# Optimization experiments

Measured on AMD Instinct MI355X. Metric: run time of the kernel, lower is better.

Reference implementation:

```python
import jax, jax.numpy as jnp
import numpy as np
from jax import lax

TAU = 1.0
LAMBDA_CONTRAST = 1.0
GAMMA_ALIGN = 1.0
EPSILON = 0.1
SINKHORN_ITERS = 50
B, V_EN, V_CN, K, H, D = 512, 30000, 20000, 100, 512, 300


def setup_inputs() -> dict:
    key = jax.random.key(0)
    ks = jax.random.split(key, 24)
    s = lambda fan_in: 1.0 / np.sqrt(fan_in)
    inp = {
        'x_bow_en': jax.random.uniform(ks[0], (B, V_EN), jnp.float32),
        'x_bow_cn': jax.random.uniform(ks[1], (B, V_CN), jnp.float32),
        'cluster_ids': jax.random.randint(ks[2], (B,), 0, 9, jnp.int32),
        'eps_en': jax.random.normal(ks[3], (B, K), jnp.float32),
        'eps_cn': jax.random.normal(ks[4], (B, K), jnp.float32),
        # English encoder params
        'W1_en': jax.random.normal(ks[5], (V_EN, H), jnp.float32) * s(V_EN),
        'b1_en': jnp.zeros((H,), jnp.float32),
        'W2_en': jax.random.normal(ks[6], (H, H), jnp.float32) * s(H),
        'b2_en': jnp.zeros((H,), jnp.float32),
        'Wmu_en': jax.random.normal(ks[7], (H, K), jnp.float32) * s(H),
        'bmu_en': jnp.zeros((K,), jnp.float32),
        'Wlv_en': jax.random.normal(ks[8], (H, K), jnp.float32) * s(H),
        'blv_en': jnp.zeros((K,), jnp.float32),
        # Chinese encoder params
        'W1_cn': jax.random.normal(ks[9], (V_CN, H), jnp.float32) * s(V_CN),
        'b1_cn': jnp.zeros((H,), jnp.float32),
        'W2_cn': jax.random.normal(ks[10], (H, H), jnp.float32) * s(H),
        'b2_cn': jnp.zeros((H,), jnp.float32),
        'Wmu_cn': jax.random.normal(ks[11], (H, K), jnp.float32) * s(H),
        'bmu_cn': jnp.zeros((K,), jnp.float32),
        'Wlv_cn': jax.random.normal(ks[12], (H, K), jnp.float32) * s(H),
        'blv_cn': jnp.zeros((K,), jnp.float32),
        # frozen word embeddings + topic embeddings
        'word_emb_en': jax.random.normal(ks[13], (V_EN, D), jnp.float32),
        'word_emb_cn': jax.random.normal(ks[14], (V_CN, D), jnp.float32),
        'topic_emb': jax.random.normal(ks[15], (K, D), jnp.float32),
    }
    return inp


def _encoder(x, eps, W1, b1, W2, b2, Wmu, bmu, Wlv, blv):
    h = jax.nn.softplus(x @ W1 + b1)
    h = jax.nn.softplus(h @ W2 + b2)
    mu = h @ Wmu + bmu
    logvar = h @ Wlv + blv
    z = mu + eps * jnp.exp(0.5 * logvar)  # reparameterization
    theta = jax.nn.softmax(z, axis=-1)
    return theta, mu, logvar


def _compute_beta(word_emb, topic_emb, tau):
    # torch.cdist p=2 -> euclidean distance [V, K]
    sq = (jnp.sum(word_emb ** 2, -1)[:, None] + jnp.sum(topic_emb ** 2, -1)[None, :]
          - 2.0 * word_emb @ topic_emb.T)
    dist = jnp.sqrt(jnp.maximum(sq, 0.0))
    beta = jnp.exp(-dist / tau)
    beta = beta / jnp.sum(beta, axis=0, keepdims=True)  # normalize over vocab
    return beta.T  # [K, V]


def _tm_loss(x_bow, theta, beta, mu, logvar):
    recon = theta @ beta  # [B, V]
    recon_loss = jnp.mean(-jnp.sum(x_bow * jax.nn.log_softmax(recon, axis=-1), axis=-1))
    kl = jnp.mean(0.5 * jnp.sum(jnp.exp(logvar) + mu ** 2 - 1.0 - logvar, axis=-1))
    return recon_loss + kl


def _contrastive_loss(theta_en, theta_cn, cluster_ids, tau):
    b = theta_en.shape[0]
    parity = (jnp.arange(b) % 2 == 0)[:, None]
    thetas = jnp.where(parity, theta_en, theta_cn)  # anchor/other selection
    tn = thetas / jnp.maximum(jnp.linalg.norm(thetas, axis=-1, keepdims=True), 1e-8)
    E = jnp.exp((tn @ tn.T) / tau)  # exp(cos_sim / tau), [B, B]
    offdiag = ~jnp.eye(b, dtype=bool)
    valid = cluster_ids > 0  # falsy cluster -> skipped, matching torch truthiness
    same = cluster_ids[:, None] == cluster_ids[None, :]
    pos_mask = offdiag & same & valid[:, None] & valid[None, :]
    pos_sim = jnp.sum(jnp.where(pos_mask, E, 0.0), axis=1)
    neg_sum = jnp.sum(jnp.where(offdiag, E, 0.0), axis=1)  # all j != i
    has_pos = valid & (jnp.sum(pos_mask, axis=1) > 0)
    per = -jnp.log(pos_sim / (pos_sim + neg_sum + 1e-8))
    loss = jnp.sum(jnp.where(has_pos, per, 0.0))
    count = jnp.sum(has_pos).astype(jnp.float32)
    return loss / (count + 1e-8)


def _sinkhorn(a, b, C, eps):
    Kmat = jnp.exp(-C / eps)
    def step(uv, _):
        u, v = uv
        u = a / (Kmat @ v + 1e-8)
        v = b / (Kmat.T @ u + 1e-8)
        return (u, v), None
    (u, v), _ = lax.scan(step, (jnp.ones_like(a), jnp.ones_like(b)), None, length=SINKHORN_ITERS)
    return u[:, None] * Kmat * v[None, :]


def _alignment_loss(topic_emb, eps):
    tn = topic_emb / jnp.maximum(jnp.linalg.norm(topic_emb, axis=-1, keepdims=True), 1e-8)
    C = 1.0 - tn @ tn.T
    k = topic_emb.shape[0]
    a = jnp.full((k,), 1.0 / k, jnp.float32)
    Q = _sinkhorn(a, a, C, eps)
    return jnp.sum(Q * C)


def reference(x_bow_en, x_bow_cn, cluster_ids, eps_en, eps_cn,
              W1_en, b1_en, W2_en, b2_en, Wmu_en, bmu_en, Wlv_en, blv_en,
              W1_cn, b1_cn, W2_cn, b2_cn, Wmu_cn, bmu_cn, Wlv_cn, blv_cn,
              word_emb_en, word_emb_cn, topic_emb):
    theta_en, mu_en, lv_en = _encoder(x_bow_en, eps_en, W1_en, b1_en, W2_en, b2_en, Wmu_en, bmu_en, Wlv_en, blv_en)
    theta_cn, mu_cn, lv_cn = _encoder(x_bow_cn, eps_cn, W1_cn, b1_cn, W2_cn, b2_cn, Wmu_cn, bmu_cn, Wlv_cn, blv_cn)
    beta_en = _compute_beta(word_emb_en, topic_emb, TAU)
    beta_cn = _compute_beta(word_emb_cn, topic_emb, TAU)
    tm_en = _tm_loss(x_bow_en, theta_en, beta_en, mu_en, lv_en)
    tm_cn = _tm_loss(x_bow_cn, theta_cn, beta_cn, mu_cn, lv_cn)
    contrast = _contrastive_loss(theta_en, theta_cn, cluster_ids, TAU)
    align = _alignment_loss(topic_emb, EPSILON)
    total = tm_en + tm_cn + LAMBDA_CONTRAST * contrast + GAMMA_ALIGN * align
    return total, tm_en, tm_cn, contrast, align, theta_en, theta_cn, beta_en, beta_cn
```

## Files before the change

### kernel.cpp

```cpp
#include <hip/hip_runtime.h>
#include <math.h>

#define BATCH 512
#define VEN 30000
#define VCN 20000
#define KT 100
#define HID 512
#define DIM 300
#define VENP 30080
#define VCNP 20096
#define KDP 320

typedef float f32x4 __attribute__((ext_vector_type(4)));
typedef short bf16x8 __attribute__((ext_vector_type(8)));
typedef unsigned short u16x8 __attribute__((ext_vector_type(8)));
typedef unsigned short u16x4 __attribute__((ext_vector_type(4)));

#define WS_H1_EN   0
#define WS_H2_EN   (WS_H1_EN + 262144)
#define WS_H1_CN   (WS_H2_EN + 262144)
#define WS_H2_CN   (WS_H1_CN + 262144)
#define WS_ROWS_EN (WS_H2_CN + 262144)
#define WS_ROWS_CN (WS_ROWS_EN + 1536)
#define WS_SCAL    (WS_ROWS_CN + 1536)
#define ZERO_FLOATS (WS_SCAL + 64)
#define WS_BIG     ZERO_FLOATS
#define XB_EN      WS_BIG
#define XB_CN      (WS_BIG + 7680000)
#define WEP_EN     WS_BIG
#define WEP_CN     (WS_BIG + 4812800)
#define TEP        (WS_BIG + 4812800 + 3215360)
#define BT_EN      (WS_BIG + 8048640)
#define BT_CN      (BT_EN + 1925120)
#define THP_EN     (BT_CN + 1286144)
#define THP_CN     (THP_EN + 32768)
#define AFTER_BIG  (WS_BIG + 12800000)
#define W1T_EN     AFTER_BIG
#define W1T_CN     (W1T_EN + 7680000)
#define W2T_EN     (W1T_CN + 5120000)
#define W2T_CN     (W2T_EN + 131072)
#define H1B_EN     (W2T_CN + 131072)
#define H1B_CN     (H1B_EN + 131072)
#define WN2_EN     (H1B_CN + 131072)
#define WN2_CN     (WN2_EN + 30080)
#define TN2        (WN2_CN + 20096)
#define WS_TNBUF   (TN2 + 128)
#define WS_TNT     (WS_TNBUF + 51200)
#define WS_CTOP    (WS_TNT + 30000)
#define WS_COLSUM_EN (WS_CTOP + 10000)
#define WS_COLSUM_CN (WS_COLSUM_EN + 128)

#define OUT_THETA_EN 5
#define OUT_THETA_CN (OUT_THETA_EN + 51200)
#define OUT_BETA_EN  (OUT_THETA_CN + 51200)
#define OUT_BETA_CN  (OUT_BETA_EN + 3000000)

__device__ __forceinline__ float waveReduceSum(float v) {
    #pragma unroll
    for (int o = 32; o > 0; o >>= 1) v += __shfl_down(v, o);
    return v;
}

__device__ __forceinline__ unsigned short f2bf(float f) {
    unsigned int u = __float_as_uint(f);
    u = (u + 0x7FFFu + ((u >> 16) & 1u)) >> 16;
    return (unsigned short)u;
}

__global__ __launch_bounds__(256)
void cast_bf16_kernel(const float* __restrict__ src, unsigned short* __restrict__ dst, int n)
{
    int i = (blockIdx.x * 256 + threadIdx.x) * 8;
    if (i < n) {
        float4 a = *(const float4*)&src[i];
        float4 b = *(const float4*)&src[i + 4];
        u16x8 o = { f2bf(a.x), f2bf(a.y), f2bf(a.z), f2bf(a.w),
                    f2bf(b.x), f2bf(b.y), f2bf(b.z), f2bf(b.w) };
        *(u16x8*)&dst[i] = o;
    }
}

template <int MODE, int AF32>
__global__ __launch_bounds__(256)
void mfma_gemm_nt(const void* __restrict__ Av, const unsigned short* __restrict__ B,
                  float* __restrict__ C, int M, int N, int K, int ldA, int ldB, int chunkK,
                  int Mreal, const float* __restrict__ an2, const float* __restrict__ bn2)
{
    __shared__ __align__(16) unsigned short As[128 * 40];
    __shared__ __align__(16) unsigned short Bs[128 * 40];
    const int tid = threadIdx.x;
    const int m0 = blockIdx.x * 128, n0 = blockIdx.y * 128;
    const int kStart = blockIdx.z * chunkK;
    const int kEnd = min(kStart + chunkK, K);

    const int wave = tid >> 6, lane = tid & 63;
    const int wm = (wave & 1) * 64, wn = (wave >> 1) * 64;
    const int l15 = lane & 15, quad = lane >> 4;

    const int srow = tid >> 1;
    const int scol = (tid & 1) * 16;

    f32x4 acc[4][4];
    #pragma unroll
    for (int i = 0; i < 4; ++i)
        #pragma unroll
        for (int j = 0; j < 4; ++j)
            acc[i][j] = (f32x4){0.f, 0.f, 0.f, 0.f};

    const u16x8 z8 = {0,0,0,0,0,0,0,0};

    for (int k0 = kStart; k0 < kEnd; k0 += 32) {
        int kA = k0 + scol;
        if (AF32) {
            const float* pa = (const float*)Av + (size_t)(m0 + srow) * ldA + kA;
            float4 f0 = {0,0,0,0}, f1 = {0,0,0,0}, f2 = {0,0,0,0}, f3 = {0,0,0,0};
            if (kA < kEnd) {
                f0 = *(const float4*)(pa);
                f1 = *(const float4*)(pa + 4);
                f2 = *(const float4*)(pa + 8);
                f3 = *(const float4*)(pa + 12);
            }
            u16x8 o0 = { f2bf(f0.x), f2bf(f0.y), f2bf(f0.z), f2bf(f0.w),
                         f2bf(f1.x), f2bf(f1.y), f2bf(f1.z), f2bf(f1.w) };
            u16x8 o1 = { f2bf(f2.x), f2bf(f2.y), f2bf(f2.z), f2bf(f2.w),
                         f2bf(f3.x), f2bf(f3.y), f2bf(f3.z), f2bf(f3.w) };
            *(u16x8*)&As[srow * 40 + scol]     = o0;
            *(u16x8*)&As[srow * 40 + scol + 8] = o1;
        } else {
            const unsigned short* pa = (const unsigned short*)Av + (size_t)(m0 + srow) * ldA + kA;
            u16x8 a0 = (kA     < kEnd) ? *(const u16x8*)(pa)     : z8;
            u16x8 a1 = (kA + 8 < kEnd) ? *(const u16x8*)(pa + 8) : z8;
            *(u16x8*)&As[srow * 40 + scol]     = a0;
            *(u16x8*)&As[srow * 40 + scol + 8] = a1;
        }
        {
            const unsigned short* pb = B + (size_t)(n0 + srow) * ldB + kA;
            u16x8 b0 = (kA     < kEnd) ? *(const u16x8*)(pb)     : z8;
            u16x8 b1 = (kA + 8 < kEnd) ? *(const u16x8*)(pb + 8) : z8;
            *(u16x8*)&Bs[srow * 40 + scol]     = b0;
            *(u16x8*)&Bs[srow * 40 + scol + 8] = b1;
        }
        __syncthreads();
        bf16x8 af[4], bfr[4];
        #pragma unroll
        for (int mi = 0; mi < 4; ++mi)
            af[mi] = *(const bf16x8*)&As[(wm + mi * 16 + l15) * 40 + quad * 8];
        #pragma unroll
        for (int ni = 0; ni < 4; ++ni)
            bfr[ni] = *(const bf16x8*)&Bs[(wn + ni * 16 + l15) * 40 + quad * 8];
        #pragma unroll
        for (int mi = 0; mi < 4; ++mi)
            #pragma unroll
            for (int ni = 0; ni < 4; ++ni)
                acc[mi][ni] = __builtin_amdgcn_mfma_f32_16x16x32_bf16(af[mi], bfr[ni], acc[mi][ni], 0, 0, 0);
        __syncthreads();
    }

    if (MODE == 0) {
        #pragma unroll
        for (int mi = 0; mi < 4; ++mi)
            #pragma unroll
            for (int ni = 0; ni < 4; ++ni)
                #pragma unroll
                for (int i = 0; i < 4; ++i) {
                    int m = m0 + wm + mi * 16 + quad * 4 + i;
                    int n = n0 + wn + ni * 16 + l15;
                    atomicAdd(&C[(size_t)m * N + n], acc[mi][ni][i]);
                }
    } else {
        #pragma unroll
        for (int mi = 0; mi < 4; ++mi)
            #pragma unroll
            for (int ni = 0; ni < 4; ++ni)
                #pragma unroll
                for (int i = 0; i < 4; ++i) {
                    int m = m0 + wm + mi * 16 + quad * 4 + i;
                    int n = n0 + wn + ni * 16 + l15;
                    if (m < Mreal && n < KT) {
                        float sq = an2[m] + bn2[n] - 2.f * acc[mi][ni][i];
                        C[(size_t)n * Mreal + m] = __expf(-sqrtf(fmaxf(sq, 0.f)));
                    }
                }
    }
}

__global__ __launch_bounds__(256)
void recon_mfma_kernel(const unsigned short* __restrict__ A, const unsigned short* __restrict__ B,
                       const float* __restrict__ x, int V, float* __restrict__ rows)
{
    __shared__ __align__(16) unsigned short As[128 * 40];
    __shared__ __align__(16) unsigned short Bs[128 * 40];
    const int tid = threadIdx.x;
    const int m0 = blockIdx.x * 128, n0 = blockIdx.y * 128;
    const int wave = tid >> 6, lane = tid & 63;
    const int wm = (wave & 1) * 64, wn = (wave >> 1) * 64;
    const int l15 = lane & 15, quad = lane >> 4;
    const int srow = tid >> 1, scol = (tid & 1) * 16;

    f32x4 acc[4][4];
    #pragma unroll
    for (int i = 0; i < 4; ++i)
        #pragma unroll
        for (int j = 0; j < 4; ++j)
            acc[i][j] = (f32x4){0.f, 0.f, 0.f, 0.f};

    for (int k0 = 0; k0 < 128; k0 += 32) {
        int kA = k0 + scol;
        *(u16x8*)&As[srow * 40 + scol]     = *(const u16x8*)(A + (size_t)(m0 + srow) * 128 + kA);
        *(u16x8*)&As[srow * 40 + scol + 8] = *(const u16x8*)(A + (size_t)(m0 + srow) * 128 + kA + 8);
        *(u16x8*)&Bs[srow * 40 + scol]     = *(const u16x8*)(B + (size_t)(n0 + srow) * 128 + kA);
        *(u16x8*)&Bs[srow * 40 + scol + 8] = *(const u16x8*)(B + (size_t)(n0 + srow) * 128 + kA + 8);
        __syncthreads();
        bf16x8 af[4], bfr[4];
        #pragma unroll
        for (int mi = 0; mi < 4; ++mi)
            af[mi] = *(const bf16x8*)&As[(wm + mi * 16 + l15) * 40 + quad * 8];
        #pragma unroll
        for (int ni = 0; ni < 4; ++ni)
            bfr[ni] = *(const bf16x8*)&Bs[(wn + ni * 16 + l15) * 40 + quad * 8];
        #pragma unroll
        for (int mi = 0; mi < 4; ++mi)
            #pragma unroll
            for (int ni = 0; ni < 4; ++ni)
                acc[mi][ni] = __builtin_amdgcn_mfma_f32_16x16x32_bf16(af[mi], bfr[ni], acc[mi][ni], 0, 0, 0);
        __syncthreads();
    }

    #pragma unroll
    for (int ni = 0; ni < 4; ++ni) {
        int b = n0 + wn + ni * 16 + l15;
        float tse = 0.f, tsxr = 0.f, tsx = 0.f;
        #pragma unroll
        for (int mi = 0; mi < 4; ++mi) {
            int v0 = m0 + wm + mi * 16 + quad * 4;
            if (v0 + 3 < V) {
                float4 xv = *(const float4*)&x[(size_t)b * V + v0];
                float xa[4] = {xv.x, xv.y, xv.z, xv.w};
                #pragma unroll
                for (int i = 0; i < 4; ++i) {
                    float r = acc[mi][ni][i];
                    tse += __expf(r);
                    tsxr += xa[i] * r;
                    tsx  += xa[i];
                }
            } else {
                #pragma unroll
                for (int i = 0; i < 4; ++i) {
                    int v = v0 + i;
                    if (v < V) {
                        float xv1 = x[(size_t)b * V + v];
                        float r = acc[mi][ni][i];
                        tse += __expf(r); tsxr += xv1 * r; tsx += xv1;
                    }
                }
            }
        }
        tse  += __shfl_xor(tse, 16);  tse  += __shfl_xor(tse, 32);
        tsxr += __shfl_xor(tsxr, 16); tsxr += __shfl_xor(tsxr, 32);
        tsx  += __shfl_xor(tsx, 16);  tsx  += __shfl_xor(tsx, 32);
        if (quad == 0) {
            atomicAdd(&rows[b], tse);
            atomicAdd(&rows[512 + b], tsxr);
            atomicAdd(&rows[1024 + b], tsx);
        }
    }
}

__global__ __launch_bounds__(256)
void transpose_cast_kernel(const float* __restrict__ src, unsigned short* __restrict__ dst,
                           int K, int N)
{
    __shared__ float tile[32][33];
    int kb = blockIdx.x * 32, nb = blockIdx.y * 32;
    int tx = threadIdx.x & 31, ty4 = threadIdx.x >> 5;
    #pragma unroll
    for (int j = 0; j < 4; ++j) {
        int k = kb + ty4 * 4 + j;
        tile[ty4 * 4 + j][tx] = (k < K) ? src[(size_t)k * N + nb + tx] : 0.f;
    }
    __syncthreads();
    #pragma unroll
    for (int j = 0; j < 4; ++j) {
        int n = nb + ty4 * 4 + j;
        int k = kb + tx;
        if (k < K) dst[(size_t)n * K + k] = f2bf(tile[tx][ty4 * 4 + j]);
    }
}

__global__ void padcast_sqnorm_kernel(const float* __restrict__ src, unsigned short* __restrict__ dst,
                                      float* __restrict__ n2, int V)
{
    int m = blockIdx.x, tid = threadIdx.x;
    float sq = 0.f;
    #pragma unroll
    for (int j = 0; j < 5; ++j) {
        int k = tid + j * 64;
        float v = (m < V && k < DIM) ? src[(size_t)m * DIM + k] : 0.f;
        dst[(size_t)m * KDP + k] = f2bf(v);
        sq += v * v;
    }
    sq = waveReduceSum(sq);
    if (tid == 0) n2[m] = sq;
}

__global__ __launch_bounds__(256)
void normbeta_bt_kernel(float* __restrict__ beta, const float* __restrict__ cs,
                        unsigned short* __restrict__ bt, int V)
{
    int v = blockIdx.x * 64 + (threadIdx.x & 63);
    int kq = threadIdx.x >> 6;
    unsigned short tmp[32];
    #pragma unroll
    for (int j = 0; j < 32; ++j) {
        int k = kq * 32 + j;
        float val = 0.f;
        if (k < KT && v < V) {
            val = beta[(size_t)k * V + v] * (1.0f / cs[k]);
            beta[(size_t)k * V + v] = val;
        }
        tmp[j] = f2bf(val);
    }
    #pragma unroll
    for (int q = 0; q < 4; ++q)
        *(u16x8*)&bt[(size_t)v * 128 + kq * 32 + q * 8] = *(u16x8*)&tmp[q * 8];
}

__global__ void theta_pad_kernel(const float* __restrict__ theta, unsigned short* __restrict__ thp)
{
    int idx = blockIdx.x * 256 + threadIdx.x;
    int b = idx >> 7, k = idx & 127;
    thp[idx] = f2bf(k < KT ? theta[b * KT + k] : 0.f);
}

__global__ __launch_bounds__(256)
void colsum_kernel(const float* __restrict__ bta, float* __restrict__ cs, int V)
{
    int k = blockIdx.x, tid = threadIdx.x;
    float s = 0.f;
    for (int v = tid; v < V; v += 256) s += bta[(size_t)k * V + v];
    s = waveReduceSum(s);
    __shared__ float cw[4];
    if ((tid & 63) == 0) cw[tid >> 6] = s;
    __syncthreads();
    if (tid == 0) cs[k] = cw[0] + cw[1] + cw[2] + cw[3];
}

__global__ void bias_softplus_bf16_kernel(const float* __restrict__ src, const float* __restrict__ b,
                                          unsigned short* __restrict__ dst, int n)
{
    int i = blockIdx.x * 256 + threadIdx.x;
    if (i < n) {
        float x = src[i] + b[i & (HID - 1)];
        float sp = fmaxf(x, 0.f) + log1pf(__expf(-fabsf(x)));
        dst[i] = f2bf(sp);
    }
}

__global__ void bias_softplus_f32_kernel(float* __restrict__ y, const float* __restrict__ b, int n)
{
    int i = blockIdx.x * 256 + threadIdx.x;
    if (i < n) {
        float x = y[i] + b[i & (HID - 1)];
        y[i] = fmaxf(x, 0.f) + log1pf(__expf(-fabsf(x)));
    }
}

__global__ __launch_bounds__(128)
void encoder_head_kernel(const float* __restrict__ h2, const float* __restrict__ Wmu,
                         const float* __restrict__ bmu, const float* __restrict__ Wlv,
                         const float* __restrict__ blv, const float* __restrict__ eps,
                         float* __restrict__ theta_out, float* __restrict__ kl_accum)
{
    int i = blockIdx.x, tid = threadIdx.x;
    __shared__ float hrow[HID];
    __shared__ float sred[128];
    #pragma unroll
    for (int j = 0; j < 4; ++j) hrow[tid + 128 * j] = h2[i * HID + tid + 128 * j];
    __syncthreads();
    float mu = 0.f, lv = 0.f;
    if (tid < KT) {
        #pragma unroll 8
        for (int h = 0; h < HID; ++h) {
            float hv = hrow[h];
            mu += hv * Wmu[h * KT + tid];
            lv += hv * Wlv[h * KT + tid];
        }
        mu += bmu[tid]; lv += blv[tid];
    }
    float z = (tid < KT) ? (mu + eps[i * KT + tid] * __expf(0.5f * lv)) : -3.0e38f;
    sred[tid] = z; __syncthreads();
    for (int s = 64; s > 0; s >>= 1) { if (tid < s) sred[tid] = fmaxf(sred[tid], sred[tid + s]); __syncthreads(); }
    float zmax = sred[0]; __syncthreads();
    float e = (tid < KT) ? __expf(z - zmax) : 0.f;
    sred[tid] = e; __syncthreads();
    for (int s = 64; s > 0; s >>= 1) { if (tid < s) sred[tid] += sred[tid + s]; __syncthreads(); }
    float esum = sred[0]; __syncthreads();
    if (tid < KT) theta_out[i * KT + tid] = e / esum;
    float kterm = (tid < KT) ? 0.5f * (__expf(lv) + mu * mu - 1.f - lv) : 0.f;
    sred[tid] = kterm; __syncthreads();
    for (int s = 64; s > 0; s >>= 1) { if (tid < s) sred[tid] += sred[tid + s]; __syncthreads(); }
    if (tid == 0) atomicAdd(kl_accum, sred[0]);
}

__global__ __launch_bounds__(256)
void recon_finalize_kernel(const float* __restrict__ rows_en, const float* __restrict__ rows_cn,
                           float* __restrict__ scal)
{
    const float* rows = (blockIdx.x == 0) ? rows_en : rows_cn;
    int tid = threadIdx.x;
    float s = 0.f;
    for (int r = tid; r < 512; r += 256) {
        float se = rows[r], sxr = rows[512 + r], sx = rows[1024 + r];
        s += __logf(se) * sx - sxr;
    }
    s = waveReduceSum(s);
    __shared__ float cw[4];
    if ((tid & 63) == 0) cw[tid >> 6] = s;
    __syncthreads();
    if (tid == 0) scal[5 + blockIdx.x] = cw[0] + cw[1] + cw[2] + cw[3];
}

__global__ __launch_bounds__(128)
void contrast_prep_kernel(const float* __restrict__ theta_en, const float* __restrict__ theta_cn,
                          float* __restrict__ tn)
{
    int i = blockIdx.x, tid = threadIdx.x;
    const float* src = ((i & 1) == 0) ? theta_en : theta_cn;
    float val = (tid < KT) ? src[i * KT + tid] : 0.f;
    __shared__ float sred[128];
    sred[tid] = val * val; __syncthreads();
    for (int s = 64; s > 0; s >>= 1) { if (tid < s) sred[tid] += sred[tid + s]; __syncthreads(); }
    float inv = 1.0f / fmaxf(sqrtf(sred[0]), 1e-8f);
    if (tid < KT) tn[i * KT + tid] = val * inv;
}

__global__ __launch_bounds__(256)
void contrast_main_kernel(const float* __restrict__ tn, const int* __restrict__ cid,
                          float* __restrict__ scal)
{
    int i = blockIdx.x, tid = threadIdx.x;
    __shared__ __align__(16) float ti[KT];
    if (tid < KT) ti[tid] = tn[i * KT + tid];
    __syncthreads();
    int ci = cid[i];
    bool vi = ci > 0;
    float pos = 0.f, neg = 0.f, pcnt = 0.f;
    for (int j = tid; j < 512; j += 256) {
        if (j == i) continue;
        float s = 0.f;
        const float4* tj = reinterpret_cast<const float4*>(&tn[j * KT]);
        #pragma unroll
        for (int q = 0; q < 25; ++q) {
            float4 t4 = tj[q];
            s += ti[4 * q] * t4.x + ti[4 * q + 1] * t4.y + ti[4 * q + 2] * t4.z + ti[4 * q + 3] * t4.w;
        }
        float E = __expf(s);
        neg += E;
        if (vi && cid[j] == ci) { pos += E; pcnt += 1.f; }
    }
    pos = waveReduceSum(pos); neg = waveReduceSum(neg); pcnt = waveReduceSum(pcnt);
    __shared__ float cw[3][4];
    int w = tid >> 6;
    if ((tid & 63) == 0) { cw[0][w] = pos; cw[1][w] = neg; cw[2][w] = pcnt; }
    __syncthreads();
    if (tid == 0) {
        float P = 0.f, N = 0.f, PC = 0.f;
        for (int q = 0; q < 4; ++q) { P += cw[0][q]; N += cw[1][q]; PC += cw[2][q]; }
        if (vi && PC > 0.f) {
            atomicAdd(&scal[2], -__logf(P / (P + N + 1e-8f)));
            atomicAdd(&scal[3], 1.0f);
        }
    }
}

__global__ void norm_rows_kernel(const float* __restrict__ A, float* __restrict__ out, int cols)
{
    int r = blockIdx.x, tid = threadIdx.x;
    float s = 0.f;
    for (int d = tid; d < cols; d += 64) { float a = A[r * cols + d]; s += a * a; }
    s = waveReduceSum(s);
    s = __shfl(s, 0);
    float inv = 1.0f / fmaxf(sqrtf(s), 1e-8f);
    for (int d = tid; d < cols; d += 64) out[r * cols + d] = A[r * cols + d] * inv;
}

__global__ __launch_bounds__(128)
void ctopic_kernel(const float* __restrict__ tnt, float* __restrict__ C)
{
    int i = blockIdx.x, tid = threadIdx.x;
    __shared__ float ti[DIM];
    for (int d = tid; d < DIM; d += 128) ti[d] = tnt[i * DIM + d];
    __syncthreads();
    for (int j = tid; j < KT; j += 128) {
        float s = 0.f;
        for (int d = 0; d < DIM; ++d) s += ti[d] * tnt[j * DIM + d];
        C[i * KT + j] = 1.0f - s;
    }
}

__global__ __launch_bounds__(128, 1)
void sinkhorn_kernel(const float* __restrict__ C, float* __restrict__ scal)
{
    __shared__ __align__(16) float ld[100 * 101];
    __shared__ __align__(16) float ub[128], vb[128];
    __shared__ float cw[2];
    const int tid = threadIdx.x;

    for (int i = tid; i < 10000; i += 128) {
        int r = i / 100, c = i - r * 100;
        ld[r * 101 + c] = C[i];
    }
    ub[tid] = 1.f; vb[tid] = 1.f;
    __syncthreads();

    float kr[100], kc[100];
    if (tid < 100) {
        #pragma unroll
        for (int j = 0; j < 100; ++j) kr[j] = __expf(-10.f * ld[tid * 101 + j]);
        #pragma unroll
        for (int j = 0; j < 100; ++j) kc[j] = __expf(-10.f * ld[j * 101 + tid]);
    }

    for (int it = 0; it < 50; ++it) {
        if (tid < 100) {
            float s = 0.f;
            #pragma unroll
            for (int q = 0; q < 25; ++q) {
                float4 v4 = *(const float4*)&vb[q * 4];
                s += kr[q*4]*v4.x + kr[q*4+1]*v4.y + kr[q*4+2]*v4.z + kr[q*4+3]*v4.w;
            }
            ub[tid] = 0.01f / (s + 1e-8f);
        }
        __syncthreads();
        if (tid < 100) {
            float s = 0.f;
            #pragma unroll
            for (int q = 0; q < 25; ++q) {
                float4 u4 = *(const float4*)&ub[q * 4];
                s += kc[q*4]*u4.x + kc[q*4+1]*u4.y + kc[q*4+2]*u4.z + kc[q*4+3]*u4.w;
            }
            vb[tid] = 0.01f / (s + 1e-8f);
        }
        __syncthreads();
    }

    float part = 0.f;
    if (tid < 100) {
        float u = ub[tid];
        #pragma unroll
        for (int q = 0; q < 25; ++q) {
            float4 v4 = *(const float4*)&vb[q * 4];
            float va[4] = {v4.x, v4.y, v4.z, v4.w};
            #pragma unroll
            for (int e = 0; e < 4; ++e) {
                int j = q * 4 + e;
                part += u * kr[j] * va[e] * ld[tid * 101 + j];
            }
        }
    }
    part = waveReduceSum(part);
    if ((tid & 63) == 0) cw[tid >> 6] = part;
    __syncthreads();
    if (tid == 0) scal[4] = cw[0] + cw[1];
}

__global__ void final_combine_kernel(const float* __restrict__ scal, float* __restrict__ out)
{
    if (threadIdx.x == 0 && blockIdx.x == 0) {
        const float invB = 1.0f / 512.0f;
        float tm_en = scal[5] * invB + scal[0] * invB;
        float tm_cn = scal[6] * invB + scal[1] * invB;
        float contrast = scal[2] / (scal[3] + 1e-8f);
        float align = scal[4];
        out[0] = tm_en + tm_cn + contrast + align;
        out[1] = tm_en;
        out[2] = tm_cn;
        out[3] = contrast;
        out[4] = align;
    }
}

extern "C" void kernel_launch(void* const* d_in, const int* in_sizes, int n_in,
                              void* d_out_v, int out_size, void* d_ws, size_t ws_size,
                              hipStream_t stream)
{
    const float* x_en   = (const float*)d_in[0];
    const float* x_cn   = (const float*)d_in[1];
    const int*   cid    = (const int*)  d_in[2];
    const float* eps_en = (const float*)d_in[3];
    const float* eps_cn = (const float*)d_in[4];
    const float* W1_en  = (const float*)d_in[5];
    const float* b1_en  = (const float*)d_in[6];
    const float* W2_en  = (const float*)d_in[7];
    const float* b2_en  = (const float*)d_in[8];
    const float* Wmu_en = (const float*)d_in[9];
    const float* bmu_en = (const float*)d_in[10];
    const float* Wlv_en = (const float*)d_in[11];
    const float* blv_en = (const float*)d_in[12];
    const float* W1_cn  = (const float*)d_in[13];
    const float* b1_cn  = (const float*)d_in[14];
    const float* W2_cn  = (const float*)d_in[15];
    const float* b2_cn  = (const float*)d_in[16];
    const float* Wmu_cn = (const float*)d_in[17];
    const float* bmu_cn = (const float*)d_in[18];
    const float* Wlv_cn = (const float*)d_in[19];
    const float* blv_cn = (const float*)d_in[20];
    const float* we_en  = (const float*)d_in[21];
    const float* we_cn  = (const float*)d_in[22];
    const float* te     = (const float*)d_in[23];
    float* out = (float*)d_out_v;
    float* ws  = (float*)d_ws;

    unsigned short* w1t_en = (unsigned short*)(ws + W1T_EN);
    unsigned short* w1t_cn = (unsigned short*)(ws + W1T_CN);
    unsigned short* w2t_en = (unsigned short*)(ws + W2T_EN);
    unsigned short* w2t_cn = (unsigned short*)(ws + W2T_CN);
    unsigned short* h1b_en = (unsigned short*)(ws + H1B_EN);
    unsigned short* h1b_cn = (unsigned short*)(ws + H1B_CN);
    unsigned short* xb_en  = (unsigned short*)(ws + XB_EN);
    unsigned short* xb_cn  = (unsigned short*)(ws + XB_CN);
    unsigned short* wep_en = (unsigned short*)(ws + WEP_EN);
    unsigned short* wep_cn = (unsigned short*)(ws + WEP_CN);
    unsigned short* tep    = (unsigned short*)(ws + TEP);
    unsigned short* bt_en  = (unsigned short*)(ws + BT_EN);
    unsigned short* bt_cn  = (unsigned short*)(ws + BT_CN);
    unsigned short* thp_en = (unsigned short*)(ws + THP_EN);
    unsigned short* thp_cn = (unsigned short*)(ws + THP_CN);

    hipMemsetAsync(d_ws, 0, (size_t)ZERO_FLOATS * sizeof(float), stream);

    cast_bf16_kernel<<<7500, 256, 0, stream>>>(x_en, xb_en, BATCH * VEN);
    cast_bf16_kernel<<<5000, 256, 0, stream>>>(x_cn, xb_cn, BATCH * VCN);

    transpose_cast_kernel<<<dim3(938, 16), 256, 0, stream>>>(W1_en, w1t_en, VEN, HID);
    transpose_cast_kernel<<<dim3(625, 16), 256, 0, stream>>>(W1_cn, w1t_cn, VCN, HID);
    transpose_cast_kernel<<<dim3(16, 16), 256, 0, stream>>>(W2_en, w2t_en, HID, HID);
    transpose_cast_kernel<<<dim3(16, 16), 256, 0, stream>>>(W2_cn, w2t_cn, HID, HID);

    mfma_gemm_nt<0, 0><<<dim3(4, 4, 32), 256, 0, stream>>>(xb_en, w1t_en, ws + WS_H1_EN,
        BATCH, HID, VEN, VEN, VEN, 960, 0, nullptr, nullptr);
    mfma_gemm_nt<0, 0><<<dim3(4, 4, 32), 256, 0, stream>>>(xb_cn, w1t_cn, ws + WS_H1_CN,
        BATCH, HID, VCN, VCN, VCN, 640, 0, nullptr, nullptr);

    bias_softplus_bf16_kernel<<<1024, 256, 0, stream>>>(ws + WS_H1_EN, b1_en, h1b_en, 262144);
    bias_softplus_bf16_kernel<<<1024, 256, 0, stream>>>(ws + WS_H1_CN, b1_cn, h1b_cn, 262144);

    mfma_gemm_nt<0, 0><<<dim3(4, 4, 8), 256, 0, stream>>>(h1b_en, w2t_en, ws + WS_H2_EN,
        BATCH, HID, HID, HID, HID, 64, 0, nullptr, nullptr);
    mfma_gemm_nt<0, 0><<<dim3(4, 4, 8), 256, 0, stream>>>(h1b_cn, w2t_cn, ws + WS_H2_CN,
        BATCH, HID, HID, HID, HID, 64, 0, nullptr, nullptr);

    bias_softplus_f32_kernel<<<1024, 256, 0, stream>>>(ws + WS_H2_EN, b2_en, 262144);
    bias_softplus_f32_kernel<<<1024, 256, 0, stream>>>(ws + WS_H2_CN, b2_cn, 262144);

    encoder_head_kernel<<<BATCH, 128, 0, stream>>>(ws + WS_H2_EN, Wmu_en, bmu_en, Wlv_en, blv_en,
                                                   eps_en, out + OUT_THETA_EN, ws + WS_SCAL + 0);
    encoder_head_kernel<<<BATCH, 128, 0, stream>>>(ws + WS_H2_CN, Wmu_cn, bmu_cn, Wlv_cn, blv_cn,
                                                   eps_cn, out + OUT_THETA_CN, ws + WS_SCAL + 1);

    padcast_sqnorm_kernel<<<VENP, 64, 0, stream>>>(we_en, wep_en, ws + WN2_EN, VEN);
    padcast_sqnorm_kernel<<<VCNP, 64, 0, stream>>>(we_cn, wep_cn, ws + WN2_CN, VCN);
    padcast_sqnorm_kernel<<<128, 64, 0, stream>>>(te, tep, ws + TN2, KT);

    mfma_gemm_nt<2, 0><<<dim3(235, 1, 1), 256, 0, stream>>>(wep_en, tep, out + OUT_BETA_EN,
        VENP, 128, KDP, KDP, KDP, KDP, VEN, ws + WN2_EN, ws + TN2);
    mfma_gemm_nt<2, 0><<<dim3(157, 1, 1), 256, 0, stream>>>(wep_cn, tep, out + OUT_BETA_CN,
        VCNP, 128, KDP, KDP, KDP, KDP, VCN, ws + WN2_CN, ws + TN2);

    colsum_kernel<<<KT, 256, 0, stream>>>(out + OUT_BETA_EN, ws + WS_COLSUM_EN, VEN);
    colsum_kernel<<<KT, 256, 0, stream>>>(out + OUT_BETA_CN, ws + WS_COLSUM_CN, VCN);

    normbeta_bt_kernel<<<VENP / 64, 256, 0, stream>>>(out + OUT_BETA_EN, ws + WS_COLSUM_EN, bt_en, VEN);
    normbeta_bt_kernel<<<VCNP / 64, 256, 0, stream>>>(out + OUT_BETA_CN, ws + WS_COLSUM_CN, bt_cn, VCN);

    theta_pad_kernel<<<256, 256, 0, stream>>>(out + OUT_THETA_EN, thp_en);
    theta_pad_kernel<<<256, 256, 0, stream>>>(out + OUT_THETA_CN, thp_cn);

    recon_mfma_kernel<<<dim3(VENP / 128, 4), 256, 0, stream>>>(bt_en, thp_en, x_en, VEN, ws + WS_ROWS_EN);
    recon_mfma_kernel<<<dim3(VCNP / 128, 4), 256, 0, stream>>>(bt_cn, thp_cn, x_cn, VCN, ws + WS_ROWS_CN);
    recon_finalize_kernel<<<2, 256, 0, stream>>>(ws + WS_ROWS_EN, ws + WS_ROWS_CN, ws + WS_SCAL);

    contrast_prep_kernel<<<BATCH, 128, 0, stream>>>(out + OUT_THETA_EN, out + OUT_THETA_CN, ws + WS_TNBUF);
    contrast_main_kernel<<<BATCH, 256, 0, stream>>>(ws + WS_TNBUF, cid, ws + WS_SCAL);

    norm_rows_kernel<<<KT, 64, 0, stream>>>(te, ws + WS_TNT, DIM);
    ctopic_kernel<<<KT, 128, 0, stream>>>(ws + WS_TNT, ws + WS_CTOP);
    sinkhorn_kernel<<<1, 128, 0, stream>>>(ws + WS_CTOP, ws + WS_SCAL);

    final_combine_kernel<<<1, 64, 0, stream>>>(ws + WS_SCAL, out);
}
```

Baseline: 894.2 us.

## Add async global-to-LDS bf16 GEMM with padded K for encoder first layer

Replaces the generic MFMA GEMM for the large first encoder layer with a dedicated kernel that loads tiles straight from global memory into LDS using global_load_lds, with XOR-swizzled LDS layout and 64-wide K steps. The input casts and W1 transposes now pad K to a multiple of 64 so the new kernel needs no bounds checks, which requires larger workspace offsets. The split-K factor for the second GEMM is also doubled. The new kernel has no double buffering and waits on all loads before compute, so load latency is not overlapped with MFMA work.

```diff
diff --git a/kernel.cpp b/kernel.cpp
--- a/kernel.cpp
+++ b/kernel.cpp
@@ -10,11 +10,13 @@
 #define VENP 30080
 #define VCNP 20096
 #define KDP 320
+#define VENK 30080
+#define VCNK 20096
 
 typedef float f32x4 __attribute__((ext_vector_type(4)));
 typedef short bf16x8 __attribute__((ext_vector_type(8)));
 typedef unsigned short u16x8 __attribute__((ext_vector_type(8)));
-typedef unsigned short u16x4 __attribute__((ext_vector_type(4)));
+typedef unsigned int u32;
 
 #define WS_H1_EN   0
 #define WS_H2_EN   (WS_H1_EN + 262144)
@@ -26,7 +28,7 @@
 #define ZERO_FLOATS (WS_SCAL + 64)
 #define WS_BIG     ZERO_FLOATS
 #define XB_EN      WS_BIG
-#define XB_CN      (WS_BIG + 7680000)
+#define XB_CN      (WS_BIG + 7700480)
 #define WEP_EN     WS_BIG
 #define WEP_CN     (WS_BIG + 4812800)
 #define TEP        (WS_BIG + 4812800 + 3215360)
@@ -34,10 +36,10 @@
 #define BT_CN      (BT_EN + 1925120)
 #define THP_EN     (BT_CN + 1286144)
 #define THP_CN     (THP_EN + 32768)
-#define AFTER_BIG  (WS_BIG + 12800000)
+#define AFTER_BIG  (WS_BIG + 12845056)
 #define W1T_EN     AFTER_BIG
-#define W1T_CN     (W1T_EN + 7680000)
-#define W2T_EN     (W1T_CN + 5120000)
+#define W1T_CN     (W1T_EN + 7700480)
+#define W2T_EN     (W1T_CN + 5144576)
 #define W2T_CN     (W2T_EN + 131072)
 #define H1B_EN     (W2T_CN + 131072)
 #define H1B_CN     (H1B_EN + 131072)
@@ -67,17 +69,97 @@
     return (unsigned short)u;
 }
 
-__global__ __launch_bounds__(256)
-void cast_bf16_kernel(const float* __restrict__ src, unsigned short* __restrict__ dst, int n)
-{
-    int i = (blockIdx.x * 256 + threadIdx.x) * 8;
-    if (i < n) {
-        float4 a = *(const float4*)&src[i];
-        float4 b = *(const float4*)&src[i + 4];
-        u16x8 o = { f2bf(a.x), f2bf(a.y), f2bf(a.z), f2bf(a.w),
-                    f2bf(b.x), f2bf(b.y), f2bf(b.z), f2bf(b.w) };
-        *(u16x8*)&dst[i] = o;
-    }
+__device__ __forceinline__ void gl2lds16(const unsigned short* g, unsigned short* l) {
+    __builtin_amdgcn_global_load_lds(
+        (const __attribute__((address_space(1))) u32*)g,
+        (__attribute__((address_space(3))) u32*)l, 16, 0, 0);
+}
+
+__global__ __launch_bounds__(256)
+void cast_pad_bf16_kernel(const float* __restrict__ src, unsigned short* __restrict__ dst,
+                          int cols, int colsPad)
+{
+    int row = blockIdx.y;
+    int col = (blockIdx.x * 256 + threadIdx.x) * 8;
+    if (col >= colsPad) return;
+    u16x8 o = {0,0,0,0,0,0,0,0};
+    if (col < cols) {
+        float4 a = *(const float4*)&src[(size_t)row * cols + col];
+        float4 b = *(const float4*)&src[(size_t)row * cols + col + 4];
+        o = (u16x8){ f2bf(a.x), f2bf(a.y), f2bf(a.z), f2bf(a.w),
+                     f2bf(b.x), f2bf(b.y), f2bf(b.z), f2bf(b.w) };
+    }
+    *(u16x8*)&dst[(size_t)row * colsPad + col] = o;
+}
+
+__global__ __launch_bounds__(256)
+void gemm1_async(const unsigned short* __restrict__ A, const unsigned short* __restrict__ B,
+                 float* __restrict__ C, int N, int ldA, int ldB, int chunkK, int K)
+{
+    __shared__ __align__(16) unsigned short As[128 * 64];
+    __shared__ __align__(16) unsigned short Bs[128 * 64];
+    const int tid = threadIdx.x;
+    const int m0 = blockIdx.x * 128, n0 = blockIdx.y * 128;
+    const int kStart = blockIdx.z * chunkK;
+    const int kEnd = min(kStart + chunkK, K);
+
+    const int wave = tid >> 6, lane = tid & 63;
+    const int wm = (wave & 1) * 64, wn = (wave >> 1) * 64;
+    const int l15 = lane & 15, quad = lane >> 4;
+
+    const int rl = lane >> 3;
+    const int cs = (lane & 7) ^ rl;
+
+    f32x4 acc[4][4];
+    #pragma unroll
+    for (int i = 0; i < 4; ++i)
+        #pragma unroll
+        for (int j = 0; j < 4; ++j)
+            acc[i][j] = (f32x4){0.f, 0.f, 0.f, 0.f};
+
+    for (int k0 = kStart; k0 < kEnd; k0 += 64) {
+        #pragma unroll
+        for (int j = 0; j < 4; ++j) {
+            int seg = wave * 4 + j;
+            int r = seg * 8 + rl;
+            gl2lds16(A + (size_t)(m0 + r) * ldA + k0 + cs * 8, &As[seg * 512]);
+            gl2lds16(B + (size_t)(n0 + r) * ldB + k0 + cs * 8, &Bs[seg * 512]);
+        }
+        asm volatile("s_waitcnt vmcnt(0)" ::: "memory");
+        __syncthreads();
+
+        #pragma unroll
+        for (int kh = 0; kh < 2; ++kh) {
+            bf16x8 af[4], bfr[4];
+            #pragma unroll
+            for (int mi = 0; mi < 4; ++mi) {
+                int r = wm + mi * 16 + l15;
+                af[mi] = *(const bf16x8*)&As[r * 64 + (((kh << 2) | quad) ^ (r & 7)) * 8];
+            }
+            #pragma unroll
+            for (int ni = 0; ni < 4; ++ni) {
+                int r = wn + ni * 16 + l15;
+                bfr[ni] = *(const bf16x8*)&Bs[r * 64 + (((kh << 2) | quad) ^ (r & 7)) * 8];
+            }
+            #pragma unroll
+            for (int mi = 0; mi < 4; ++mi)
+                #pragma unroll
+                for (int ni = 0; ni < 4; ++ni)
+                    acc[mi][ni] = __builtin_amdgcn_mfma_f32_16x16x32_bf16(af[mi], bfr[ni], acc[mi][ni], 0, 0, 0);
+        }
+        __syncthreads();
+    }
+
+    #pragma unroll
+    for (int mi = 0; mi < 4; ++mi)
+        #pragma unroll
+        for (int ni = 0; ni < 4; ++ni)
+            #pragma unroll
+            for (int i = 0; i < 4; ++i) {
+                int m = m0 + wm + mi * 16 + quad * 4 + i;
+                int n = n0 + wn + ni * 16 + l15;
+                atomicAdd(&C[(size_t)m * N + n], acc[mi][ni][i]);
+            }
 }
 
 template <int MODE, int AF32>
@@ -268,7 +350,7 @@
 
 __global__ __launch_bounds__(256)
 void transpose_cast_kernel(const float* __restrict__ src, unsigned short* __restrict__ dst,
-                           int K, int N)
+                           int K, int N, int Kp)
 {
     __shared__ float tile[32][33];
     int kb = blockIdx.x * 32, nb = blockIdx.y * 32;
@@ -283,7 +365,7 @@
     for (int j = 0; j < 4; ++j) {
         int n = nb + ty4 * 4 + j;
         int k = kb + tx;
-        if (k < K) dst[(size_t)n * K + k] = f2bf(tile[tx][ty4 * 4 + j]);
+        if (k < Kp) dst[(size_t)n * Kp + k] = f2bf(tile[tx][ty4 * 4 + j]);
     }
 }
 
@@ -629,26 +711,26 @@
 
     hipMemsetAsync(d_ws, 0, (size_t)ZERO_FLOATS * sizeof(float), stream);
 
-    cast_bf16_kernel<<<7500, 256, 0, stream>>>(x_en, xb_en, BATCH * VEN);
-    cast_bf16_kernel<<<5000, 256, 0, stream>>>(x_cn, xb_cn, BATCH * VCN);
-
-    transpose_cast_kernel<<<dim3(938, 16), 256, 0, stream>>>(W1_en, w1t_en, VEN, HID);
-    transpose_cast_kernel<<<dim3(625, 16), 256, 0, stream>>>(W1_cn, w1t_cn, VCN, HID);
-    transpose_cast_kernel<<<dim3(16, 16), 256, 0, stream>>>(W2_en, w2t_en, HID, HID);
-    transpose_cast_kernel<<<dim3(16, 16), 256, 0, stream>>>(W2_cn, w2t_cn, HID, HID);
-
-    mfma_gemm_nt<0, 0><<<dim3(4, 4, 32), 256, 0, stream>>>(xb_en, w1t_en, ws + WS_H1_EN,
-        BATCH, HID, VEN, VEN, VEN, 960, 0, nullptr, nullptr);
-    mfma_gemm_nt<0, 0><<<dim3(4, 4, 32), 256, 0, stream>>>(xb_cn, w1t_cn, ws + WS_H1_CN,
-        BATCH, HID, VCN, VCN, VCN, 640, 0, nullptr, nullptr);
+    cast_pad_bf16_kernel<<<dim3(15, 512), 256, 0, stream>>>(x_en, xb_en, VEN, VENK);
+    cast_pad_bf16_kernel<<<dim3(10, 512), 256, 0, stream>>>(x_cn, xb_cn, VCN, VCNK);
+
+    transpose_cast_kernel<<<dim3(940, 16), 256, 0, stream>>>(W1_en, w1t_en, VEN, HID, VENK);
+    transpose_cast_kernel<<<dim3(628, 16), 256, 0, stream>>>(W1_cn, w1t_cn, VCN, HID, VCNK);
+    transpose_cast_kernel<<<dim3(16, 16), 256, 0, stream>>>(W2_en, w2t_en, HID, HID, HID);
+    transpose_cast_kernel<<<dim3(16, 16), 256, 0, stream>>>(W2_cn, w2t_cn, HID, HID, HID);
+
+    gemm1_async<<<dim3(4, 4, 47), 256, 0, stream>>>(xb_en, w1t_en, ws + WS_H1_EN,
+        HID, VENK, VENK, 640, VENK);
+    gemm1_async<<<dim3(4, 4, 32), 256, 0, stream>>>(xb_cn, w1t_cn, ws + WS_H1_CN,
+        HID, VCNK, VCNK, 640, VCNK);
 
     bias_softplus_bf16_kernel<<<1024, 256, 0, stream>>>(ws + WS_H1_EN, b1_en, h1b_en, 262144);
     bias_softplus_bf16_kernel<<<1024, 256, 0, stream>>>(ws + WS_H1_CN, b1_cn, h1b_cn, 262144);
 
-    mfma_gemm_nt<0, 0><<<dim3(4, 4, 8), 256, 0, stream>>>(h1b_en, w2t_en, ws + WS_H2_EN,
-        BATCH, HID, HID, HID, HID, 64, 0, nullptr, nullptr);
-    mfma_gemm_nt<0, 0><<<dim3(4, 4, 8), 256, 0, stream>>>(h1b_cn, w2t_cn, ws + WS_H2_CN,
-        BATCH, HID, HID, HID, HID, 64, 0, nullptr, nullptr);
+    mfma_gemm_nt<0, 0><<<dim3(4, 4, 16), 256, 0, stream>>>(h1b_en, w2t_en, ws + WS_H2_EN,
+        BATCH, HID, HID, HID, HID, 32, 0, nullptr, nullptr);
+    mfma_gemm_nt<0, 0><<<dim3(4, 4, 16), 256, 0, stream>>>(h1b_cn, w2t_cn, ws + WS_H2_CN,
+        BATCH, HID, HID, HID, HID, 32, 0, nullptr, nullptr);
 
     bias_softplus_f32_kernel<<<1024, 256, 0, stream>>>(ws + WS_H2_EN, b2_en, 262144);
     bias_softplus_f32_kernel<<<1024, 256, 0, stream>>>(ws + WS_H2_CN, b2_cn, 262144);
```

Measured after the change: 891.2 us. About the same (-0.3%).
